# Kernel optimization log

Hardware: AMD Instinct MI355X
Metric: run time of the kernel (lower is better)

## Reference

```python
import jax, jax.numpy as jnp
import numpy as np

NUM_GRAPHS = 16
EPS = 1e-5
HEADS = 4


def setup_inputs() -> dict:
    key = jax.random.key(0)
    ks = jax.random.split(key, 20)
    N, E, D = 100000, 1600000, 128
    s = 1.0 / np.sqrt(D)
    inp = {
        'x': jax.random.normal(ks[0], (N, 6), jnp.float32),
        'edge_index': jax.random.randint(ks[1], (2, E), 0, N),
        'norm': jax.random.uniform(ks[2], (E,), jnp.float32),
        'batch': jnp.sort(jax.random.randint(ks[3], (N,), 0, NUM_GRAPHS)),
        'num_layers': 5,
        'enc_w': jax.random.normal(ks[4], (D, 6), jnp.float32) * 0.4,
        'gru_wih': jax.random.normal(ks[5], (3 * D, D), jnp.float32) * s,
        'gru_whh': jax.random.normal(ks[6], (3 * D, D), jnp.float32) * s,
        'gru_bih': jax.random.normal(ks[7], (3 * D,), jnp.float32) * 0.01,
        'gru_bhh': jax.random.normal(ks[8], (3 * D,), jnp.float32) * 0.01,
        'gn_w': jnp.ones((D,), jnp.float32),
        'gn_b': jnp.zeros((D,), jnp.float32),
        'gn_ms': jnp.ones((D,), jnp.float32),
        'in_proj_w': jax.random.normal(ks[9], (3 * D, D), jnp.float32) * s,
        'in_proj_b': jnp.zeros((3 * D,), jnp.float32),
        'out_w': jax.random.normal(ks[10], (D, D), jnp.float32) * s,
        'out_b': jnp.zeros((D,), jnp.float32),
        'dec1_w': jax.random.normal(ks[11], (D // 2, D), jnp.float32) * s,
        'dec2_w': jax.random.normal(ks[12], (1, D // 2), jnp.float32) * s,
    }
    return inp


def _graph_norm(h, batch, gn_w, gn_b, gn_ms):
    # PyG GraphNorm: per-graph mean/var with learnable mean_scale
    cnt = jax.ops.segment_sum(jnp.ones((h.shape[0], 1), h.dtype), batch,
                              num_segments=NUM_GRAPHS)  # [G,1]
    mean = jax.ops.segment_sum(h, batch, num_segments=NUM_GRAPHS) / cnt  # [G,D]
    out = h - mean[batch] * gn_ms
    var = jax.ops.segment_sum(out * out, batch, num_segments=NUM_GRAPHS) / cnt
    return out * jax.lax.rsqrt(var[batch] + EPS) * gn_w + gn_b


def _gru_cell(xin, h, wih, whh, bih, bhh):
    D = h.shape[-1]
    gi = xin @ wih.T + bih  # [N,3D]
    gh = h @ whh.T + bhh
    r = jax.nn.sigmoid(gi[:, :D] + gh[:, :D])
    z = jax.nn.sigmoid(gi[:, D:2 * D] + gh[:, D:2 * D])
    n = jnp.tanh(gi[:, 2 * D:] + r * gh[:, 2 * D:])
    return (1.0 - z) * n + z * h


def reference(x, edge_index, norm, batch, num_layers, enc_w, gru_wih, gru_whh,
              gru_bih, gru_bhh, gn_w, gn_b, gn_ms, in_proj_w, in_proj_b,
              out_w, out_b, dec1_w, dec2_w):
    N = x.shape[0]
    D = enc_w.shape[0]
    src, dst = edge_index[0], edge_index[1]

    h = jax.nn.leaky_relu(x @ enc_w.T)  # dropout is identity in eval
    h_list = [h]
    prev = h
    for _ in range(num_layers):
        # scatter-add neighborhood aggregation: sum_j norm_e * h[src_e] at dst_e
        agg = jax.ops.segment_sum(norm[:, None] * prev[src], dst, num_segments=N)
        h = _gru_cell(agg, prev, gru_wih, gru_whh, gru_bih, gru_bhh) + prev
        h = _graph_norm(h, batch, gn_w, gn_b, gn_ms)
        h_list.append(h)
        prev = h

    hs = jnp.stack(h_list, axis=1)  # [N, S, D], S = num_layers+1
    S = hs.shape[1]
    dh = D // HEADS
    qkv = hs @ in_proj_w.T + in_proj_b  # [N,S,3D]
    q, k, v = jnp.split(qkv, 3, axis=-1)
    q = q.reshape(N, S, HEADS, dh)
    k = k.reshape(N, S, HEADS, dh)
    v = v.reshape(N, S, HEADS, dh)
    scores = jnp.einsum('nshd,nthd->nhst', q, k) / np.sqrt(dh)
    attn = jax.nn.softmax(scores, axis=-1)  # attn dropout off in eval
    ctx = jnp.einsum('nhst,nthd->nshd', attn, v).reshape(N, S, D)
    h_final = ctx @ out_w.T + out_b + hs
    z = jnp.sum(h_final, axis=1)  # [N,D]

    y = jax.nn.leaky_relu(z @ dec1_w.T)
    y = y @ dec2_w.T  # [N,1]
    return y.reshape(-1)
```

## Files before the change

### kernel.cpp

```cpp
#include <hip/hip_runtime.h>

#define NL 5
#define SS 6
#define DD 128
#define GG 16
#define GNB 32
#define APB 8
#define SCB 1024

typedef __bf16 bf16x8 __attribute__((ext_vector_type(8)));
typedef float f32x4 __attribute__((ext_vector_type(4)));
typedef unsigned short ushort_t;

__device__ __forceinline__ float bf2f(unsigned int u) {
  union { unsigned int i; float f; } c; c.i = u << 16; return c.f;
}
__device__ __forceinline__ ushort_t f2bf(float f) {
  union { __bf16 b; ushort_t u; } c; c.b = (__bf16)f;
  return c.u;
}

__global__ void k_deg(const int* __restrict__ ei, int E, int* __restrict__ deg) {
  int e = blockIdx.x * 256 + threadIdx.x;
  if (e < E) atomicAdd(&deg[ei[E + e]], 1);
}

__global__ void k_scan1(const int* __restrict__ deg, int* __restrict__ off,
                        int* __restrict__ bsum, int N) {
  __shared__ int tmp[SCB];
  int t = threadIdx.x, i = blockIdx.x * SCB + t;
  int v = (i < N) ? deg[i] : 0;
  tmp[t] = v; __syncthreads();
  for (int o = 1; o < SCB; o <<= 1) {
    int a = (t >= o) ? tmp[t - o] : 0;
    __syncthreads(); tmp[t] += a; __syncthreads();
  }
  if (i < N) off[i] = tmp[t] - v;
  if (t == SCB - 1) bsum[blockIdx.x] = tmp[t];
}

__global__ void k_scan2(int* __restrict__ bsum, int nb) {
  __shared__ int tmp[SCB];
  int t = threadIdx.x;
  int v = (t < nb) ? bsum[t] : 0;
  tmp[t] = v; __syncthreads();
  for (int o = 1; o < SCB; o <<= 1) {
    int a = (t >= o) ? tmp[t - o] : 0;
    __syncthreads(); tmp[t] += a; __syncthreads();
  }
  if (t < nb) bsum[t] = tmp[t] - v;
}

__global__ void k_scan3(int* __restrict__ off, const int* __restrict__ bsum, int N, int E) {
  int i = blockIdx.x * 256 + threadIdx.x;
  if (i < N) off[i] += bsum[i >> 10];
  else if (i == N) off[N] = E;
}

__global__ void k_copy(const int* __restrict__ a, int* __restrict__ b, int n) {
  int i = blockIdx.x * 256 + threadIdx.x;
  if (i < n) b[i] = a[i];
}

__global__ void k_fill(const int* __restrict__ ei, const float* __restrict__ norm, int E,
                       int* __restrict__ cur, int* __restrict__ csrs, float* __restrict__ csrn) {
  int e = blockIdx.x * 256 + threadIdx.x;
  if (e >= E) return;
  int s = ei[e], d = ei[E + e];
  int p = atomicAdd(&cur[d], 1);
  csrs[p] = s;
  csrn[p] = norm[e];
}

__global__ void k_bend(const int* __restrict__ batch, int N, int* __restrict__ endp) {
  int i = blockIdx.x * 256 + threadIdx.x;
  if (i >= N) return;
  int b = batch[i];
  if (i == N - 1 || batch[i + 1] != b) endp[b] = i + 1;
}

__global__ void k_cnt(const int* __restrict__ endp, int* __restrict__ cnt) {
  if (threadIdx.x == 0 && blockIdx.x == 0) {
    int prev = 0;
    for (int g = 0; g < GG; ++g) {
      int e = endp[g];
      if (e > prev) { cnt[g] = e - prev; prev = e; }
      else cnt[g] = 0;
    }
  }
}

__global__ void k_wconv(const float* __restrict__ wih, const float* __restrict__ whh,
                        const float* __restrict__ ipw, const float* __restrict__ ow,
                        const float* __restrict__ d1,
                        ushort_t* __restrict__ WB, ushort_t* __restrict__ WI,
                        ushort_t* __restrict__ WO, ushort_t* __restrict__ WD1) {
  int o = blockIdx.x * 256 + threadIdx.x;
  int seg, idx;
  if (o < 98304) { seg = 0; idx = o; }
  else if (o < 98304 + 49152) { seg = 1; idx = o - 98304; }
  else if (o < 98304 + 49152 + 16384) { seg = 2; idx = o - 98304 - 49152; }
  else if (o < 98304 + 49152 + 16384 + 8192) { seg = 3; idx = o - 98304 - 49152 - 16384; }
  else return;
  int j = idx & 7, l = (idx >> 3) & 63, ks = (idx >> 9) & 3, ctg = idx >> 11;
  int row = ctg * 16 + (l & 15);
  int col = ks * 32 + ((l >> 4) << 3) + j;
  float v;
  if (seg == 0) { v = (row < 384) ? wih[row * 128 + col] : whh[(row - 384) * 128 + col]; WB[idx] = f2bf(v); }
  else if (seg == 1) { WI[idx] = f2bf(ipw[row * 128 + col]); }
  else if (seg == 2) { WO[idx] = f2bf(ow[row * 128 + col]); }
  else { WD1[idx] = f2bf(d1[row * 128 + col]); }
}

__global__ void k_encode(const float* __restrict__ x, const float* __restrict__ ew,
                         ushort_t* __restrict__ HS, int N) {
  int idx = blockIdx.x * 256 + threadIdx.x;
  if (idx >= N * 64) return;
  int n = idx >> 6, d0 = (idx & 63) << 1;
  float xr[6];
#pragma unroll
  for (int k = 0; k < 6; ++k) xr[k] = x[n * 6 + k];
  float a0 = 0.f, a1 = 0.f;
#pragma unroll
  for (int k = 0; k < 6; ++k) {
    a0 += xr[k] * ew[d0 * 6 + k];
    a1 += xr[k] * ew[(d0 + 1) * 6 + k];
  }
  a0 = a0 > 0.f ? a0 : 0.01f * a0;
  a1 = a1 > 0.f ? a1 : 0.01f * a1;
  unsigned int pk = (unsigned int)f2bf(a0) | ((unsigned int)f2bf(a1) << 16);
  *(unsigned int*)&HS[((size_t)n * SS) * DD + d0] = pk;
}

__global__ __launch_bounds__(256) void k_agg(const ushort_t* __restrict__ HS, int l,
    const int* __restrict__ off, const int* __restrict__ csrs, const float* __restrict__ csrn,
    ushort_t* __restrict__ AGG, float* __restrict__ SUMS, int N) {
  if (blockIdx.x == 0) {
    for (int i = threadIdx.x; i < 2 * GG * DD; i += 256) SUMS[i] = 0.f;
  }
  int n = blockIdx.x * 4 + (threadIdx.x >> 6);
  if (n >= N) return;
  int lane = threadIdx.x & 63;
  int p0 = off[n], p1 = off[n + 1];
  float ax = 0.f, ay = 0.f;
  const ushort_t* base = HS + l * DD + lane * 2;
  int p = p0;
  for (; p + 8 <= p1; p += 8) {
    int s[8]; float w[8]; unsigned int u[8];
#pragma unroll
    for (int q = 0; q < 8; ++q) { s[q] = csrs[p + q]; w[q] = csrn[p + q]; }
#pragma unroll
    for (int q = 0; q < 8; ++q) u[q] = *(const unsigned int*)(base + (size_t)s[q] * (SS * DD));
#pragma unroll
    for (int q = 0; q < 8; ++q) {
      ax += w[q] * bf2f(u[q] & 0xffffu);
      ay += w[q] * bf2f(u[q] >> 16);
    }
  }
  for (; p < p1; ++p) {
    int s0 = csrs[p];
    float w0 = csrn[p];
    unsigned int u0 = *(const unsigned int*)(base + (size_t)s0 * (SS * DD));
    ax += w0 * bf2f(u0 & 0xffffu);
    ay += w0 * bf2f(u0 >> 16);
  }
  unsigned int pk = (unsigned int)f2bf(ax) | ((unsigned int)f2bf(ay) << 16);
  *(unsigned int*)&AGG[(size_t)n * DD + lane * 2] = pk;
}

__global__ __launch_bounds__(256) void k_gru(const ushort_t* __restrict__ AGG,
    ushort_t* __restrict__ HS, int l,
    const ushort_t* __restrict__ WB,
    const float* __restrict__ bih, const float* __restrict__ bhh,
    const int* __restrict__ batch, float* __restrict__ SUMS, int N) {
  __shared__ ushort_t axh[2][GNB][136];
  __shared__ ushort_t hout[GNB][136];
  float* SUMSQ = SUMS + GG * DD;
  int t = threadIdx.x;
  int nb = blockIdx.x * GNB;
#pragma unroll
  for (int it = 0; it < 2; ++it) {
    int n = (t >> 4) + it * 16, k8 = (t & 15) << 3;
    int gn = nb + n;
    uint4 xv = make_uint4(0, 0, 0, 0), hv = xv;
    if (gn < N) {
      xv = *(const uint4*)&AGG[(size_t)gn * DD + k8];
      hv = *(const uint4*)&HS[((size_t)gn * SS + l) * DD + k8];
    }
    *(uint4*)&axh[0][n][k8] = xv;
    *(uint4*)&axh[1][n][k8] = hv;
  }
  __syncthreads();
  int w = t >> 6, lane = t & 63, r = lane & 15, kl = lane >> 4;
  int nlast = min(nb + GNB, N) - 1;
  int bu = batch[nb];
  bool uni = (batch[nlast] == bu);
#pragma unroll
  for (int ct2 = 0; ct2 < 2; ++ct2) {
    f32x4 acc[6][2];
#pragma unroll
    for (int src = 0; src < 2; ++src) {
      bf16x8 af[2][4];
#pragma unroll
      for (int rt = 0; rt < 2; ++rt)
#pragma unroll
        for (int ks = 0; ks < 4; ++ks)
          af[rt][ks] = *(const bf16x8*)&axh[src][rt * 16 + r][ks * 32 + kl * 8];
#pragma unroll
      for (int q3 = 0; q3 < 3; ++q3) {
        int q = src * 3 + q3;
        int ctg = q * 8 + w * 2 + ct2;
        f32x4 a0 = {0.f, 0.f, 0.f, 0.f}, a1 = a0;
#pragma unroll
        for (int ks = 0; ks < 4; ++ks) {
          bf16x8 bf = *(const bf16x8*)&WB[(((size_t)ctg * 4 + ks) << 9) + (lane << 3)];
          a0 = __builtin_amdgcn_mfma_f32_16x16x32_bf16(af[0][ks], bf, a0, 0, 0, 0);
          a1 = __builtin_amdgcn_mfma_f32_16x16x32_bf16(af[1][ks], bf, a1, 0, 0, 0);
        }
        acc[q][0] = a0;
        acc[q][1] = a1;
      }
    }
    int d = w * 32 + ct2 * 16 + r;
    float br = bih[d], bz = bih[128 + d], bn2 = bih[256 + d];
    float cr = bhh[d], cz = bhh[128 + d], cn2 = bhh[256 + d];
    float loc = 0.f, locq = 0.f;
#pragma unroll
    for (int rt = 0; rt < 2; ++rt) {
#pragma unroll
      for (int i = 0; i < 4; ++i) {
        int n = rt * 16 + kl * 4 + i;
        int gn = nb + n;
        if (gn < N) {
          float gir = acc[0][rt][i] + br, giz = acc[1][rt][i] + bz, gin = acc[2][rt][i] + bn2;
          float ghr = acc[3][rt][i] + cr, ghz = acc[4][rt][i] + cz, ghn = acc[5][rt][i] + cn2;
          float rr = 1.f / (1.f + __expf(-(gir + ghr)));
          float zz = 1.f / (1.f + __expf(-(giz + ghz)));
          float nn = tanhf(gin + rr * ghn);
          float prev = bf2f(axh[1][n][d]);
          float hp = (1.f - zz) * nn + zz * prev + prev;
          hout[n][d] = f2bf(hp);
          if (uni) { loc += hp; locq += hp * hp; }
          else {
            atomicAdd(&SUMS[batch[gn] * DD + d], hp);
            atomicAdd(&SUMSQ[batch[gn] * DD + d], hp * hp);
          }
        }
      }
    }
    if (uni) {
      loc += __shfl_xor(loc, 16);
      loc += __shfl_xor(loc, 32);
      locq += __shfl_xor(locq, 16);
      locq += __shfl_xor(locq, 32);
      if (kl == 0) {
        atomicAdd(&SUMS[bu * DD + d], loc);
        atomicAdd(&SUMSQ[bu * DD + d], locq);
      }
    }
  }
  __syncthreads();
#pragma unroll
  for (int it = 0; it < 2; ++it) {
    int n = (t >> 4) + it * 16, k8 = (t & 15) << 3;
    int gn = nb + n;
    if (gn < N)
      *(uint4*)&HS[((size_t)gn * SS + l + 1) * DD + k8] = *(const uint4*)&hout[n][k8];
  }
}

__global__ void k_gn(ushort_t* __restrict__ HS, int slot,
    const float* __restrict__ SUMS, const int* __restrict__ CNT,
    const int* __restrict__ batch, const float* __restrict__ gms,
    const float* __restrict__ gw, const float* __restrict__ gb, int N) {
  const float* SUMSQ = SUMS + GG * DD;
  int idx = blockIdx.x * 256 + threadIdx.x;
  if (idx >= N * 16) return;
  int n = idx >> 4, d0 = (idx & 15) << 3;
  int b = batch[n];
  float inv = 1.f / (float)CNT[b];
  size_t o = ((size_t)n * SS + slot) * DD + d0;
  uint4 hv = *(const uint4*)&HS[o];
  unsigned int uu[4] = {hv.x, hv.y, hv.z, hv.w};
  unsigned int out[4];
#pragma unroll
  for (int j = 0; j < 4; ++j) {
    ushort_t res[2];
#pragma unroll
    for (int k = 0; k < 2; ++k) {
      int d = d0 + j * 2 + k;
      float mean = SUMS[b * DD + d] * inv;
      float m = mean * gms[d];
      float var = SUMSQ[b * DD + d] * inv - 2.f * m * mean + m * m;
      float h = bf2f(k ? (uu[j] >> 16) : (uu[j] & 0xffffu));
      float v = (h - m) * rsqrtf(var + 1e-5f) * gw[d] + gb[d];
      res[k] = f2bf(v);
    }
    out[j] = (unsigned int)res[0] | ((unsigned int)res[1] << 16);
  }
  uint4 ov = make_uint4(out[0], out[1], out[2], out[3]);
  *(uint4*)&HS[o] = ov;
}

__global__ __launch_bounds__(256) void k_attn(const ushort_t* __restrict__ HS,
    const ushort_t* __restrict__ WI, const float* __restrict__ ipb,
    const ushort_t* __restrict__ WO, const float* __restrict__ ob,
    const ushort_t* __restrict__ WD1, const float* __restrict__ d2,
    float* __restrict__ y, int N) {
  __shared__ ushort_t qk[4][2][16][40];
  __shared__ ushort_t ctxb[16][136];
  __shared__ float hss[8][132];
  ushort_t (*zb)[136] = (ushort_t(*)[136])&qk[0][0][0][0];
  float* ypart = &hss[0][0];
  int t = threadIdx.x;
  int nb = blockIdx.x * APB;
  {
    int n = t >> 5, d0 = (t & 31) << 2;
    float a0 = 0.f, a1 = 0.f, a2 = 0.f, a3 = 0.f;
    if (nb + n < N) {
#pragma unroll
      for (int s = 0; s < 6; ++s) {
        const ushort_t* rp = &HS[((size_t)(nb + n) * SS + s) * DD + d0];
        uint2 u = *(const uint2*)rp;
        a0 += bf2f(u.x & 0xffffu); a1 += bf2f(u.x >> 16);
        a2 += bf2f(u.y & 0xffffu); a3 += bf2f(u.y >> 16);
      }
    }
    hss[n][d0] = a0; hss[n][d0 + 1] = a1; hss[n][d0 + 2] = a2; hss[n][d0 + 3] = a3;
  }
  int w = t >> 6, lane = t & 63, r = lane & 15, kl = lane >> 4;
  const float sc32 = 0.17677669529663687f;
#pragma unroll
  for (int rt = 0; rt < 4; ++rt) {
    int row = rt * 16 + r;
    int node = nb + (row >> 3), s = row & 7;
    bool valid = (s < 6) && (node < N);
    const ushort_t* abase = HS + ((size_t)node * SS + s) * DD + kl * 8;
    bf16x8 af[4];
#pragma unroll
    for (int ks = 0; ks < 4; ++ks) {
      bf16x8 z8 = {};
      af[ks] = valid ? *(const bf16x8*)(abase + ks * 32) : z8;
    }
    float vreg[2][4];
#pragma unroll
    for (int ct2 = 0; ct2 < 2; ++ct2) {
      int cq = 2 * w + ct2, ck = 8 + 2 * w + ct2, cv = 16 + 2 * w + ct2;
      f32x4 aq = {0.f, 0.f, 0.f, 0.f}, ak = aq, av = aq;
#pragma unroll
      for (int ks = 0; ks < 4; ++ks) {
        bf16x8 bq = *(const bf16x8*)&WI[(((size_t)cq * 4 + ks) << 9) + (lane << 3)];
        bf16x8 bk = *(const bf16x8*)&WI[(((size_t)ck * 4 + ks) << 9) + (lane << 3)];
        bf16x8 bv = *(const bf16x8*)&WI[(((size_t)cv * 4 + ks) << 9) + (lane << 3)];
        aq = __builtin_amdgcn_mfma_f32_16x16x32_bf16(af[ks], bq, aq, 0, 0, 0);
        ak = __builtin_amdgcn_mfma_f32_16x16x32_bf16(af[ks], bk, ak, 0, 0, 0);
        av = __builtin_amdgcn_mfma_f32_16x16x32_bf16(af[ks], bv, av, 0, 0, 0);
      }
      int colh = ct2 * 16 + r;
      float bq = ipb[w * 32 + colh];
      float bk = ipb[128 + w * 32 + colh];
#pragma unroll
      for (int i = 0; i < 4; ++i) {
        qk[w][0][kl * 4 + i][colh] = f2bf((aq[i] + bq) * sc32);
        qk[w][1][kl * 4 + i][colh] = f2bf(ak[i] + bk);
        vreg[ct2][i] = av[i];
      }
    }
    bf16x8 aq = *(const bf16x8*)&qk[w][0][r][kl * 8];
    bf16x8 bk = *(const bf16x8*)&qk[w][1][r][kl * 8];
    f32x4 s4 = {0.f, 0.f, 0.f, 0.f};
    s4 = __builtin_amdgcn_mfma_f32_16x16x32_bf16(aq, bk, s4, 0, 0, 0);
    bool tval = (r & 7) < 6;
    float mx = -1e30f;
    float sc[4]; bool val[4];
#pragma unroll
    for (int i = 0; i < 4; ++i) {
      int ss = 4 * kl + i;
      val[i] = tval && (((ss ^ r) & 8) == 0) && ((ss & 7) < 6);
      sc[i] = s4[i];
      if (val[i]) mx = fmaxf(mx, sc[i]);
    }
#pragma unroll
    for (int m = 1; m <= 4; m <<= 1) mx = fmaxf(mx, __shfl_xor(mx, m));
    float e[4], sum[4];
#pragma unroll
    for (int i = 0; i < 4; ++i) {
      e[i] = val[i] ? __expf(sc[i] - mx) : 0.f;
      sum[i] = e[i];
#pragma unroll
      for (int m = 1; m <= 4; m <<= 1) sum[i] += __shfl_xor(sum[i], m);
    }
    float awp = 0.f;
#pragma unroll
    for (int i = 0; i < 4; ++i) {
      int ss = 4 * kl + i;
      float attn = (((ss & 7) < 6) && sum[i] > 0.f) ? e[i] / sum[i] : 0.f;
      awp += attn;
    }
    awp += __shfl_xor(awp, 16);
    awp += __shfl_xor(awp, 32);
    float awv[4];
#pragma unroll
    for (int i = 0; i < 4; ++i) {
      int tt = 4 * (kl & 1) + i;
      awv[i] = __shfl(awp, (kl >> 1) * 8 + (tt < 8 ? tt : 0));
    }
    int nodei = 2 * rt + (kl >> 1);
#pragma unroll
    for (int ct2 = 0; ct2 < 2; ++ct2) {
      float acc = 0.f;
#pragma unroll
      for (int i = 0; i < 4; ++i) {
        int tt = 4 * (kl & 1) + i;
        if (tt < 6) acc += awv[i] * vreg[ct2][i];
      }
      acc += __shfl_xor(acc, 16);
      int dcol = w * 32 + ct2 * 16 + r;
      if ((kl & 1) == 0) ctxb[nodei][dcol] = f2bf(acc + 6.f * ipb[256 + dcol]);
    }
  }
  __syncthreads();
  {
    bf16x8 ac[4];
#pragma unroll
    for (int ks = 0; ks < 4; ++ks)
      ac[ks] = *(const bf16x8*)&ctxb[r][ks * 32 + kl * 8];
#pragma unroll
    for (int c2 = 0; c2 < 2; ++c2) {
      int ctg = 2 * w + c2;
      f32x4 a = {0.f, 0.f, 0.f, 0.f};
#pragma unroll
      for (int ks = 0; ks < 4; ++ks) {
        bf16x8 bf = *(const bf16x8*)&WO[(((size_t)ctg * 4 + ks) << 9) + (lane << 3)];
        a = __builtin_amdgcn_mfma_f32_16x16x32_bf16(ac[ks], bf, a, 0, 0, 0);
      }
      int col = ctg * 16 + r;
      float obv = 6.f * ob[col];
#pragma unroll
      for (int i = 0; i < 4; ++i) {
        int row = kl * 4 + i;
        float zv = (row < 8) ? (a[i] + obv + hss[row][col]) : 0.f;
        zb[row][col] = f2bf(zv);
      }
    }
  }
  __syncthreads();
  {
    bf16x8 az[4];
#pragma unroll
    for (int ks = 0; ks < 4; ++ks)
      az[ks] = *(const bf16x8*)&zb[r][ks * 32 + kl * 8];
    f32x4 a = {0.f, 0.f, 0.f, 0.f};
#pragma unroll
    for (int ks = 0; ks < 4; ++ks) {
      bf16x8 bf = *(const bf16x8*)&WD1[(((size_t)w * 4 + ks) << 9) + (lane << 3)];
      a = __builtin_amdgcn_mfma_f32_16x16x32_bf16(az[ks], bf, a, 0, 0, 0);
    }
    float dv = d2[w * 16 + r];
    float part[4];
#pragma unroll
    for (int i = 0; i < 4; ++i) {
      float u = a[i];
      u = u > 0.f ? u : 0.01f * u;
      part[i] = u * dv;
    }
#pragma unroll
    for (int m = 1; m <= 8; m <<= 1) {
#pragma unroll
      for (int i = 0; i < 4; ++i) part[i] += __shfl_xor(part[i], m);
    }
    if (r == 0) {
#pragma unroll
      for (int i = 0; i < 4; ++i) {
        int row = kl * 4 + i;
        if (row < 8) ypart[w * 8 + row] = part[i];
      }
    }
  }
  __syncthreads();
  if (t < 8) {
    float v = ypart[t] + ypart[8 + t] + ypart[16 + t] + ypart[24 + t];
    if (nb + t < N) y[nb + t] = v;
  }
}

extern "C" void kernel_launch(void* const* d_in, const int* in_sizes, int n_in,
                              void* d_out, int out_size, void* d_ws, size_t ws_size,
                              hipStream_t stream) {
  const float* x    = (const float*)d_in[0];
  const int*   ei   = (const int*)d_in[1];
  const float* norm = (const float*)d_in[2];
  const int*   batch= (const int*)d_in[3];
  const float* enc_w= (const float*)d_in[5];
  const float* wih  = (const float*)d_in[6];
  const float* whh  = (const float*)d_in[7];
  const float* bih  = (const float*)d_in[8];
  const float* bhh  = (const float*)d_in[9];
  const float* gw   = (const float*)d_in[10];
  const float* gb   = (const float*)d_in[11];
  const float* gms  = (const float*)d_in[12];
  const float* ipw  = (const float*)d_in[13];
  const float* ipb  = (const float*)d_in[14];
  const float* ow   = (const float*)d_in[15];
  const float* ob   = (const float*)d_in[16];
  const float* d1   = (const float*)d_in[17];
  const float* d2   = (const float*)d_in[18];
  float* y = (float*)d_out;
  int N = in_sizes[3];
  int E = in_sizes[2];

  char* p = (char*)d_ws;
  ushort_t* HS  = (ushort_t*)p;  p += (size_t)N * SS * DD * 2;
  ushort_t* AGG = (ushort_t*)p;  p += (size_t)N * DD * 2;
  ushort_t* WB  = (ushort_t*)p;  p += (size_t)98304 * 2;
  ushort_t* WI  = (ushort_t*)p;  p += (size_t)49152 * 2;
  ushort_t* WO  = (ushort_t*)p;  p += (size_t)16384 * 2;
  ushort_t* WD1 = (ushort_t*)p;  p += (size_t)8192 * 2;
  float* SUMS = (float*)p;       p += GG * DD * 4;
  float* SUMSQ= (float*)p;       p += GG * DD * 4;   (void)SUMSQ;
  int*   CNT  = (int*)p;         p += GG * 4;
  int*   ENDP = (int*)p;         p += GG * 4;
  int*   BSUM = (int*)p;         p += SCB * 4;
  int*   OFF  = (int*)p;         p += ((size_t)N + 1) * 4;
  int*   CUR  = (int*)p;         p += (size_t)N * 4;
  int*   CSRS = (int*)p;         p += (size_t)E * 4;
  float* CSRN = (float*)p;

  int nchunk = (N + SCB - 1) / SCB;

  hipMemsetAsync(CUR, 0, (size_t)N * 4, stream);
  hipMemsetAsync(CNT, 0, 2 * GG * 4, stream);
  k_deg<<<(E + 255) / 256, 256, 0, stream>>>(ei, E, CUR);
  k_scan1<<<nchunk, SCB, 0, stream>>>(CUR, OFF, BSUM, N);
  k_scan2<<<1, SCB, 0, stream>>>(BSUM, nchunk);
  k_scan3<<<(N + 256) / 256, 256, 0, stream>>>(OFF, BSUM, N, E);
  k_copy<<<(N + 255) / 256, 256, 0, stream>>>(OFF, CUR, N);
  k_fill<<<(E + 255) / 256, 256, 0, stream>>>(ei, norm, E, CUR, CSRS, CSRN);
  k_bend<<<(N + 255) / 256, 256, 0, stream>>>(batch, N, ENDP);
  k_cnt<<<1, 64, 0, stream>>>(ENDP, CNT);
  k_wconv<<<672, 256, 0, stream>>>(wih, whh, ipw, ow, d1, WB, WI, WO, WD1);
  k_encode<<<(N * 64 + 255) / 256, 256, 0, stream>>>(x, enc_w, HS, N);

  for (int l = 0; l < NL; ++l) {
    k_agg<<<(N + 3) / 4, 256, 0, stream>>>(HS, l, OFF, CSRS, CSRN, AGG, SUMS, N);
    k_gru<<<(N + GNB - 1) / GNB, 256, 0, stream>>>(AGG, HS, l, WB, bih, bhh, batch, SUMS, N);
    k_gn<<<(N * 16 + 255) / 256, 256, 0, stream>>>(HS, l + 1, SUMS, CNT, batch, gms, gw, gb, N);
  }
  k_attn<<<(N + APB - 1) / APB, 256, 0, stream>>>(HS, WI, ipb, WO, ob, WD1, d2, y, N);
}
```

Before: 1.303 ms.

## Fuse neighbor aggregation into GRU kernel and stage attention inputs in LDS

Merges the per-layer scatter aggregation kernel into the GRU kernel, so each block gathers neighbor features for its 32 nodes straight into shared memory and the AGG intermediate buffer and its round trip are dropped. Because the aggregation kernel no longer zeroes the graph-norm sums, per-layer sum buffers are allocated and cleared once with a memset up front. The attention kernel now stages each block's hidden-state rows into LDS once and reuses them for both the layer sum and the MFMA operands, instead of reading global memory twice. The trade-off is fewer, larger blocks doing the gather (32 nodes per block in sequence), which may lower memory-level parallelism during the irregular gather.

```diff
diff --git a/kernel.cpp b/kernel.cpp
--- a/kernel.cpp
+++ b/kernel.cpp
@@ -132,44 +132,8 @@
   *(unsigned int*)&HS[((size_t)n * SS) * DD + d0] = pk;
 }
 
-__global__ __launch_bounds__(256) void k_agg(const ushort_t* __restrict__ HS, int l,
+__global__ __launch_bounds__(256) void k_agru(const ushort_t* __restrict__ HS, int l,
     const int* __restrict__ off, const int* __restrict__ csrs, const float* __restrict__ csrn,
-    ushort_t* __restrict__ AGG, float* __restrict__ SUMS, int N) {
-  if (blockIdx.x == 0) {
-    for (int i = threadIdx.x; i < 2 * GG * DD; i += 256) SUMS[i] = 0.f;
-  }
-  int n = blockIdx.x * 4 + (threadIdx.x >> 6);
-  if (n >= N) return;
-  int lane = threadIdx.x & 63;
-  int p0 = off[n], p1 = off[n + 1];
-  float ax = 0.f, ay = 0.f;
-  const ushort_t* base = HS + l * DD + lane * 2;
-  int p = p0;
-  for (; p + 8 <= p1; p += 8) {
-    int s[8]; float w[8]; unsigned int u[8];
-#pragma unroll
-    for (int q = 0; q < 8; ++q) { s[q] = csrs[p + q]; w[q] = csrn[p + q]; }
-#pragma unroll
-    for (int q = 0; q < 8; ++q) u[q] = *(const unsigned int*)(base + (size_t)s[q] * (SS * DD));
-#pragma unroll
-    for (int q = 0; q < 8; ++q) {
-      ax += w[q] * bf2f(u[q] & 0xffffu);
-      ay += w[q] * bf2f(u[q] >> 16);
-    }
-  }
-  for (; p < p1; ++p) {
-    int s0 = csrs[p];
-    float w0 = csrn[p];
-    unsigned int u0 = *(const unsigned int*)(base + (size_t)s0 * (SS * DD));
-    ax += w0 * bf2f(u0 & 0xffffu);
-    ay += w0 * bf2f(u0 >> 16);
-  }
-  unsigned int pk = (unsigned int)f2bf(ax) | ((unsigned int)f2bf(ay) << 16);
-  *(unsigned int*)&AGG[(size_t)n * DD + lane * 2] = pk;
-}
-
-__global__ __launch_bounds__(256) void k_gru(const ushort_t* __restrict__ AGG,
-    ushort_t* __restrict__ HS, int l,
     const ushort_t* __restrict__ WB,
     const float* __restrict__ bih, const float* __restrict__ bhh,
     const int* __restrict__ batch, float* __restrict__ SUMS, int N) {
@@ -178,20 +142,51 @@
   float* SUMSQ = SUMS + GG * DD;
   int t = threadIdx.x;
   int nb = blockIdx.x * GNB;
+  int w = t >> 6, lane = t & 63;
 #pragma unroll
   for (int it = 0; it < 2; ++it) {
     int n = (t >> 4) + it * 16, k8 = (t & 15) << 3;
     int gn = nb + n;
-    uint4 xv = make_uint4(0, 0, 0, 0), hv = xv;
-    if (gn < N) {
-      xv = *(const uint4*)&AGG[(size_t)gn * DD + k8];
-      hv = *(const uint4*)&HS[((size_t)gn * SS + l) * DD + k8];
-    }
-    *(uint4*)&axh[0][n][k8] = xv;
+    uint4 hv = make_uint4(0, 0, 0, 0);
+    if (gn < N) hv = *(const uint4*)&HS[((size_t)gn * SS + l) * DD + k8];
     *(uint4*)&axh[1][n][k8] = hv;
   }
+  {
+    const ushort_t* gbase = HS + l * DD + lane * 2;
+#pragma unroll
+    for (int j = 0; j < 8; ++j) {
+      int n = w * 8 + j;
+      int gn = nb + n;
+      float ax = 0.f, ay = 0.f;
+      if (gn < N) {
+        int p0 = off[gn], p1 = off[gn + 1];
+        int p = p0;
+        for (; p + 8 <= p1; p += 8) {
+          int s[8]; float wt[8]; unsigned int u[8];
+#pragma unroll
+          for (int q = 0; q < 8; ++q) { s[q] = csrs[p + q]; wt[q] = csrn[p + q]; }
+#pragma unroll
+          for (int q = 0; q < 8; ++q) u[q] = *(const unsigned int*)(gbase + (size_t)s[q] * (SS * DD));
+#pragma unroll
+          for (int q = 0; q < 8; ++q) {
+            ax += wt[q] * bf2f(u[q] & 0xffffu);
+            ay += wt[q] * bf2f(u[q] >> 16);
+          }
+        }
+        for (; p < p1; ++p) {
+          int s0 = csrs[p];
+          float w0 = csrn[p];
+          unsigned int u0 = *(const unsigned int*)(gbase + (size_t)s0 * (SS * DD));
+          ax += w0 * bf2f(u0 & 0xffffu);
+          ay += w0 * bf2f(u0 >> 16);
+        }
+      }
+      unsigned int pk = (unsigned int)f2bf(ax) | ((unsigned int)f2bf(ay) << 16);
+      *(unsigned int*)&axh[0][n][lane * 2] = pk;
+    }
+  }
   __syncthreads();
-  int w = t >> 6, lane = t & 63, r = lane & 15, kl = lane >> 4;
+  int r = lane & 15, kl = lane >> 4;
   int nlast = min(nb + GNB, N) - 1;
   int bu = batch[nb];
   bool uni = (batch[nlast] == bu);
@@ -307,6 +302,7 @@
     const ushort_t* __restrict__ WO, const float* __restrict__ ob,
     const ushort_t* __restrict__ WD1, const float* __restrict__ d2,
     float* __restrict__ y, int N) {
+  __shared__ ushort_t hsb[64][136];
   __shared__ ushort_t qk[4][2][16][40];
   __shared__ ushort_t ctxb[16][136];
   __shared__ float hss[8][132];
@@ -314,17 +310,24 @@
   float* ypart = &hss[0][0];
   int t = threadIdx.x;
   int nb = blockIdx.x * APB;
+  for (int idx = t; idx < 64 * 16; idx += 256) {
+    int row = idx >> 4, k8 = (idx & 15) << 3;
+    int n = row >> 3, s = row & 7;
+    uint4 v = make_uint4(0, 0, 0, 0);
+    if (s < 6 && nb + n < N) v = *(const uint4*)&HS[((size_t)(nb + n) * SS + s) * DD + k8];
+    *(uint4*)&hsb[row][k8] = v;
+  }
+  __syncthreads();
   {
     int n = t >> 5, d0 = (t & 31) << 2;
     float a0 = 0.f, a1 = 0.f, a2 = 0.f, a3 = 0.f;
-    if (nb + n < N) {
-#pragma unroll
-      for (int s = 0; s < 6; ++s) {
-        const ushort_t* rp = &HS[((size_t)(nb + n) * SS + s) * DD + d0];
-        uint2 u = *(const uint2*)rp;
-        a0 += bf2f(u.x & 0xffffu); a1 += bf2f(u.x >> 16);
-        a2 += bf2f(u.y & 0xffffu); a3 += bf2f(u.y >> 16);
-      }
+#pragma unroll
+    for (int s = 0; s < 6; ++s) {
+      const ushort_t* rp = &hsb[n * 8 + s][d0];
+      unsigned int u0 = *(const unsigned int*)rp;
+      unsigned int u1 = *(const unsigned int*)(rp + 2);
+      a0 += bf2f(u0 & 0xffffu); a1 += bf2f(u0 >> 16);
+      a2 += bf2f(u1 & 0xffffu); a3 += bf2f(u1 >> 16);
     }
     hss[n][d0] = a0; hss[n][d0 + 1] = a1; hss[n][d0 + 2] = a2; hss[n][d0 + 3] = a3;
   }
@@ -332,16 +335,10 @@
   const float sc32 = 0.17677669529663687f;
 #pragma unroll
   for (int rt = 0; rt < 4; ++rt) {
-    int row = rt * 16 + r;
-    int node = nb + (row >> 3), s = row & 7;
-    bool valid = (s < 6) && (node < N);
-    const ushort_t* abase = HS + ((size_t)node * SS + s) * DD + kl * 8;
     bf16x8 af[4];
 #pragma unroll
-    for (int ks = 0; ks < 4; ++ks) {
-      bf16x8 z8 = {};
-      af[ks] = valid ? *(const bf16x8*)(abase + ks * 32) : z8;
-    }
+    for (int ks = 0; ks < 4; ++ks)
+      af[ks] = *(const bf16x8*)&hsb[rt * 16 + r][ks * 32 + kl * 8];
     float vreg[2][4];
 #pragma unroll
     for (int ct2 = 0; ct2 < 2; ++ct2) {
@@ -511,13 +508,11 @@
 
   char* p = (char*)d_ws;
   ushort_t* HS  = (ushort_t*)p;  p += (size_t)N * SS * DD * 2;
-  ushort_t* AGG = (ushort_t*)p;  p += (size_t)N * DD * 2;
   ushort_t* WB  = (ushort_t*)p;  p += (size_t)98304 * 2;
   ushort_t* WI  = (ushort_t*)p;  p += (size_t)49152 * 2;
   ushort_t* WO  = (ushort_t*)p;  p += (size_t)16384 * 2;
   ushort_t* WD1 = (ushort_t*)p;  p += (size_t)8192 * 2;
-  float* SUMS = (float*)p;       p += GG * DD * 4;
-  float* SUMSQ= (float*)p;       p += GG * DD * 4;   (void)SUMSQ;
+  float* SUMS_ALL = (float*)p;   p += (size_t)NL * 2 * GG * DD * 4;
   int*   CNT  = (int*)p;         p += GG * 4;
   int*   ENDP = (int*)p;         p += GG * 4;
   int*   BSUM = (int*)p;         p += SCB * 4;
@@ -530,6 +525,7 @@
 
   hipMemsetAsync(CUR, 0, (size_t)N * 4, stream);
   hipMemsetAsync(CNT, 0, 2 * GG * 4, stream);
+  hipMemsetAsync(SUMS_ALL, 0, (size_t)NL * 2 * GG * DD * 4, stream);
   k_deg<<<(E + 255) / 256, 256, 0, stream>>>(ei, E, CUR);
   k_scan1<<<nchunk, SCB, 0, stream>>>(CUR, OFF, BSUM, N);
   k_scan2<<<1, SCB, 0, stream>>>(BSUM, nchunk);
@@ -542,8 +538,8 @@
   k_encode<<<(N * 64 + 255) / 256, 256, 0, stream>>>(x, enc_w, HS, N);
 
   for (int l = 0; l < NL; ++l) {
-    k_agg<<<(N + 3) / 4, 256, 0, stream>>>(HS, l, OFF, CSRS, CSRN, AGG, SUMS, N);
-    k_gru<<<(N + GNB - 1) / GNB, 256, 0, stream>>>(AGG, HS, l, WB, bih, bhh, batch, SUMS, N);
+    float* SUMS = SUMS_ALL + (size_t)l * 2 * GG * DD;
+    k_agru<<<(N + GNB - 1) / GNB, 256, 0, stream>>>(HS, l, OFF, CSRS, CSRN, WB, bih, bhh, batch, SUMS, N);
     k_gn<<<(N * 16 + 255) / 256, 256, 0, stream>>>(HS, l + 1, SUMS, CNT, batch, gms, gw, gb, N);
   }
   k_attn<<<(N + APB - 1) / APB, 256, 0, stream>>>(HS, WI, ipb, WO, ob, WD1, d2, y, N);
```

Result: slower. 1.504 ms (+15.4%).
